# Performance work log

Hardware: AMD Instinct MI355X
Metric: run time of the kernel (lower is better)

The kernel has to match this reference:

```python
import jax, jax.numpy as jnp
import numpy as np

DIM = 1024
HEADS = 16
DIM_HEAD = 64
NUM_KV_HEADS = 4
INNER = HEADS * DIM_HEAD          # 1024
KV_DIM = NUM_KV_HEADS * DIM_HEAD  # 256
SCALE = DIM_HEAD ** -0.5


def setup_inputs() -> dict:
    key = jax.random.key(0)
    ks = jax.random.split(key, 7)
    B, S = 2, 2048
    x = jax.random.normal(ks[0], (B, S, DIM), dtype=jnp.float32)
    init = lambda k, shape: jax.random.normal(k, shape, dtype=jnp.float32) * (shape[0] ** -0.5)
    return {
        "x": x,
        "ln_gamma": jnp.ones((DIM,), jnp.float32),
        "ln_beta": jnp.zeros((DIM,), jnp.float32),
        "w_q": init(ks[1], (DIM, INNER)),
        "w_k": init(ks[2], (DIM, KV_DIM)),
        "w_v": init(ks[3], (DIM, KV_DIM)),
        "w_o": init(ks[4], (INNER, DIM)),
        "b_o": jnp.zeros((DIM,), jnp.float32),
    }


def reference(x, ln_gamma, ln_beta, w_q, w_k, w_v, w_o, b_o):
    B, S, _ = x.shape
    g, hpg, d = NUM_KV_HEADS, HEADS // NUM_KV_HEADS, DIM_HEAD
    # LayerNorm (eps matches torch default 1e-5)
    mu = jnp.mean(x, axis=-1, keepdims=True)
    var = jnp.mean((x - mu) ** 2, axis=-1, keepdims=True)
    xn = (x - mu) * jax.lax.rsqrt(var + 1e-5) * ln_gamma + ln_beta
    # projections
    q = xn @ w_q  # [B,S,INNER]
    k = xn @ w_k  # [B,S,KV_DIM]
    v = xn @ w_v
    # q: b s (g hpg d) -> b g hpg s d  (head index h = g*hpg + i, g-major)
    q = q.reshape(B, S, g, hpg, d).transpose(0, 2, 3, 1, 4)
    k = k.reshape(B, S, g, d).transpose(0, 2, 1, 3)  # [B,g,S,d]
    v = v.reshape(B, S, g, d).transpose(0, 2, 1, 3)
    dots = jnp.einsum('bghqd,bgkd->bghqk', q, k) * SCALE
    attn = jax.nn.softmax(dots, axis=-1)
    out = jnp.einsum('bghqk,bgkd->bghqd', attn, v)
    # b g hpg s d -> b s (g hpg d)
    out = out.transpose(0, 3, 1, 2, 4).reshape(B, S, INNER)
    return out @ w_o + b_o
```

## Files before the change

### kernel.cpp

```cpp
#include <hip/hip_runtime.h>

typedef unsigned short u16;
typedef __bf16 bf16x8 __attribute__((ext_vector_type(8)));
typedef short s16x4 __attribute__((ext_vector_type(4)));
typedef float f32x4 __attribute__((ext_vector_type(4)));

__device__ __forceinline__ unsigned f2u(float f) { union { float f; unsigned u; } v; v.f = f; return v.u; }
__device__ __forceinline__ float u2f(unsigned u) { union { unsigned u; float f; } v; v.u = u; return v.f; }

__device__ __forceinline__ u16 f32_to_bf16(float f) {
  unsigned u = f2u(f);
  return (u16)((u + 0x7FFFu + ((u >> 16) & 1u)) >> 16);
}
__device__ __forceinline__ unsigned pack_rnd(float a, float b) {
  unsigned ra = f2u(a), rb = f2u(b);
  ra = ra + 0x7FFFu + ((ra >> 16) & 1u);
  rb = (rb + 0x7FFFu + ((rb >> 16) & 1u)) & 0xFFFF0000u;
  return (ra >> 16) | rb;
}
__device__ __forceinline__ unsigned pack_trunc(float a, float b) {
#if __has_builtin(__builtin_amdgcn_perm)
  return __builtin_amdgcn_perm(f2u(b), f2u(a), 0x07060302u);
#else
  return (f2u(a) >> 16) | (f2u(b) & 0xFFFF0000u);
#endif
}
__device__ __forceinline__ unsigned perm_lo(unsigned a, unsigned b) {
#if __has_builtin(__builtin_amdgcn_perm)
  return __builtin_amdgcn_perm(b, a, 0x05040100u);
#else
  return (a & 0xFFFFu) | (b << 16);
#endif
}
__device__ __forceinline__ unsigned perm_hi(unsigned a, unsigned b) {
#if __has_builtin(__builtin_amdgcn_perm)
  return __builtin_amdgcn_perm(b, a, 0x07060302u);
#else
  return (a >> 16) | (b & 0xFFFF0000u);
#endif
}

#if __has_builtin(__builtin_amdgcn_global_load_lds)
#define ASYNC_CP 1
typedef __attribute__((address_space(1))) const unsigned gu32;
typedef __attribute__((address_space(3))) unsigned lu32;
__device__ __forceinline__ void gl_lds16(const u16* g, u16* l) {
  __builtin_amdgcn_global_load_lds((gu32*)g, (lu32*)l, 16, 0, 0);
}
#else
#define ASYNC_CP 0
#endif

__global__ __launch_bounds__(256) void prep_kernel(
    const float* __restrict__ x, const float* __restrict__ gamma,
    const float* __restrict__ beta, u16* __restrict__ xn,
    const float* __restrict__ w_q, const float* __restrict__ w_k,
    const float* __restrict__ w_v, const float* __restrict__ w_o,
    u16* __restrict__ wqkvT, u16* __restrict__ woT) {
  __shared__ float tile[64][65];
  int t = threadIdx.x;
  int bid = blockIdx.x;
  if (bid < 4096) {
    int row = bid;
    const float4 v = ((const float4*)(x + (size_t)row * 1024))[t];
    float s = v.x + v.y + v.z + v.w;
    float ss = v.x * v.x + v.y * v.y + v.z * v.z + v.w * v.w;
#pragma unroll
    for (int m = 1; m < 64; m <<= 1) {
      s += __shfl_xor(s, m, 64);
      ss += __shfl_xor(ss, m, 64);
    }
    __shared__ float as_[4], ass[4];
    int wave = t >> 6;
    if ((t & 63) == 0) { as_[wave] = s; ass[wave] = ss; }
    __syncthreads();
    s = as_[0] + as_[1] + as_[2] + as_[3];
    ss = ass[0] + ass[1] + ass[2] + ass[3];
    float mu = s * (1.0f / 1024.0f);
    float var = ss * (1.0f / 1024.0f) - mu * mu;
    float rstd = rsqrtf(var + 1e-5f);
    float4 g = ((const float4*)gamma)[t];
    float4 b = ((const float4*)beta)[t];
    uint2 o;
    o.x = pack_rnd((v.x - mu) * rstd * g.x + b.x, (v.y - mu) * rstd * g.y + b.y);
    o.y = pack_rnd((v.z - mu) * rstd * g.z + b.z, (v.w - mu) * rstd * g.w + b.w);
    ((uint2*)(xn + (size_t)row * 1024))[t] = o;
    return;
  }
  int idx = bid - 4096;
  const float* src; u16* dst; int N, n0, k0;
  if (idx < 256) {
    src = w_q; dst = wqkvT; N = 1024; n0 = (idx & 15) * 64; k0 = (idx >> 4) * 64;
  } else if (idx < 320) {
    int i = idx - 256;
    src = w_k; dst = wqkvT + 1024 * 1024; N = 256; n0 = (i & 3) * 64; k0 = (i >> 2) * 64;
  } else if (idx < 384) {
    int i = idx - 320;
    src = w_v; dst = wqkvT + 1280 * 1024; N = 256; n0 = (i & 3) * 64; k0 = (i >> 2) * 64;
  } else {
    int i = idx - 384;
    src = w_o; dst = woT; N = 1024; n0 = (i & 15) * 64; k0 = (i >> 4) * 64;
  }
  const int K = 1024;
  int c = t & 63, r4 = t >> 6;
#pragma unroll
  for (int rr = r4; rr < 64; rr += 4)
    tile[rr][c] = src[(size_t)(k0 + rr) * N + n0 + c];
  __syncthreads();
#pragma unroll
  for (int rr = r4; rr < 64; rr += 4)
    dst[(size_t)(n0 + rr) * K + k0 + c] = f32_to_bf16(tile[c][rr]);
}

template <int OUT_MODE>
__global__ __launch_bounds__(256) void gemm_bf16_k(
    const u16* __restrict__ A, const u16* __restrict__ Bt,
    void* __restrict__ Cv, const float* __restrict__ bias,
    int M, int N, int K, int ldc, float qscale, int qcols) {
  __shared__ __align__(16) u16 sA[64 * 64];
  __shared__ __align__(16) u16 sB[128 * 64];
  int t = threadIdx.x;
  int m0 = blockIdx.y * 64, n0 = blockIdx.x * 128;
  int wave = t >> 6, lane = t & 63;
  int wm = wave >> 1, wn = wave & 1;
  int l15 = lane & 15, quad = lane >> 4;

  f32x4 acc[2][4];
#pragma unroll
  for (int i = 0; i < 2; i++)
#pragma unroll
    for (int j = 0; j < 4; j++) acc[i][j] = f32x4{0.f, 0.f, 0.f, 0.f};

  int arow = wave * 8 + (lane >> 3);
  int achk = (lane & 7) * 8;
  const u16* Ap = A + (size_t)(m0 + arow) * K + achk;
  const u16* Bp = Bt + (size_t)(n0 + arow) * K + achk;
  u16* sAw = &sA[(wave * 8) * 64];
  u16* sBw = &sB[(wave * 8) * 64];

  for (int k0 = 0; k0 < K; k0 += 64) {
#if ASYNC_CP
    __syncthreads();
    gl_lds16(Ap + k0, sAw);
    gl_lds16(Ap + k0 + (size_t)32 * K, sAw + 32 * 64);
    gl_lds16(Bp + k0, sBw);
    gl_lds16(Bp + k0 + (size_t)32 * K, sBw + 32 * 64);
    gl_lds16(Bp + k0 + (size_t)64 * K, sBw + 64 * 64);
    gl_lds16(Bp + k0 + (size_t)96 * K, sBw + 96 * 64);
    __syncthreads();
#else
    uint4 av0 = *(const uint4*)(Ap + k0);
    uint4 av1 = *(const uint4*)(Ap + k0 + (size_t)32 * K);
    uint4 bv0 = *(const uint4*)(Bp + k0);
    uint4 bv1 = *(const uint4*)(Bp + k0 + (size_t)32 * K);
    uint4 bv2 = *(const uint4*)(Bp + k0 + (size_t)64 * K);
    uint4 bv3 = *(const uint4*)(Bp + k0 + (size_t)96 * K);
    __syncthreads();
    *(uint4*)&sA[arow * 64 + achk] = av0;
    *(uint4*)&sA[(arow + 32) * 64 + achk] = av1;
    *(uint4*)&sB[arow * 64 + achk] = bv0;
    *(uint4*)&sB[(arow + 32) * 64 + achk] = bv1;
    *(uint4*)&sB[(arow + 64) * 64 + achk] = bv2;
    *(uint4*)&sB[(arow + 96) * 64 + achk] = bv3;
    __syncthreads();
#endif
#pragma unroll
    for (int ks = 0; ks < 2; ++ks) {
      bf16x8 af[2], bf[4];
#pragma unroll
      for (int mi = 0; mi < 2; mi++)
        af[mi] = *(const bf16x8*)&sA[(wm * 32 + mi * 16 + l15) * 64 + ks * 32 + quad * 8];
#pragma unroll
      for (int ni = 0; ni < 4; ni++)
        bf[ni] = *(const bf16x8*)&sB[(wn * 64 + ni * 16 + l15) * 64 + ks * 32 + quad * 8];
#pragma unroll
      for (int mi = 0; mi < 2; mi++)
#pragma unroll
        for (int ni = 0; ni < 4; ni++)
          acc[mi][ni] = __builtin_amdgcn_mfma_f32_16x16x32_bf16(
              af[mi], bf[ni], acc[mi][ni], 0, 0, 0);
    }
  }
#pragma unroll
  for (int mi = 0; mi < 2; mi++)
#pragma unroll
    for (int ni = 0; ni < 4; ni++) {
      int row = m0 + wm * 32 + mi * 16 + quad * 4;
      int col = n0 + wn * 64 + ni * 16 + l15;
#pragma unroll
      for (int rr = 0; rr < 4; rr++) {
        float vv = acc[mi][ni][rr];
        if (OUT_MODE == 0) {
          float sc = (col < qcols) ? qscale : 1.0f;
          ((u16*)Cv)[(size_t)(row + rr) * ldc + col] = f32_to_bf16(vv * sc);
        } else {
          ((float*)Cv)[(size_t)(row + rr) * ldc + col] = vv + bias[col];
        }
      }
    }
}

__global__ __launch_bounds__(256) void attn_kernel(
    const u16* __restrict__ qkv, u16* __restrict__ oP0, u16* __restrict__ oP1,
    float* __restrict__ lP0, float* __restrict__ lP1) {
  const int LD = 1536;
  int qt = blockIdx.x;
  int bh = blockIdx.y;
  int kz = blockIdx.z;
  int b = bh >> 4, h = bh & 15, g = h >> 2;
  u16* oP = kz ? oP1 : oP0;
  float* lP = kz ? lP1 : lP0;

  __shared__ __align__(16) u16 sK[64 * 72];
  __shared__ __align__(16) u16 sV[64 * 72];

  int t = threadIdx.x, wave = t >> 6, lane = t & 63;
  int l15 = lane & 15, quad = lane >> 4;

  const u16* qbase = qkv + (size_t)(b * 2048 + qt * 256 + wave * 64) * LD + h * 64;
  const u16* kbase = qkv + (size_t)(b * 2048 + kz * 1024) * LD + 1024 + g * 64;
  const u16* vbase = kbase + 256;

  bf16x8 qf[4][2];
#pragma unroll
  for (int qs = 0; qs < 4; ++qs)
#pragma unroll
    for (int ks = 0; ks < 2; ++ks)
      qf[qs][ks] = *(const bf16x8*)(qbase + (size_t)(qs * 16 + l15) * LD + ks * 32 + quad * 8);

  f32x4 oacc[4][4];
  f32x4 lacc[4];
#pragma unroll
  for (int qs = 0; qs < 4; ++qs) {
    lacc[qs] = f32x4{0.f, 0.f, 0.f, 0.f};
#pragma unroll
    for (int md = 0; md < 4; ++md) oacc[qs][md] = f32x4{0.f, 0.f, 0.f, 0.f};
  }

  const s16x4 ones = {(short)0x3F80, (short)0x3F80, (short)0x3F80, (short)0x3F80};
  const f32x4 fzero = {0.f, 0.f, 0.f, 0.f};

  int sr = t >> 3, sq = t & 7;
  int vkp = (t & 31) * 2, vdc = (t >> 5) * 8;

  uint4 ka0, ka1, va0, va1;
  {
    const u16* kp0 = kbase + (size_t)sr * LD + sq * 8;
    ka0 = *(const uint4*)kp0;
    ka1 = *(const uint4*)(kp0 + (size_t)32 * LD);
    const u16* vp0 = vbase + (size_t)vkp * LD + vdc;
    va0 = *(const uint4*)vp0;
    va1 = *(const uint4*)(vp0 + LD);
  }

  for (int kt = 0; kt < 16; ++kt) {
    __syncthreads();
    *(uint4*)&sK[sr * 72 + sq * 8] = ka0;
    *(uint4*)&sK[(sr + 32) * 72 + sq * 8] = ka1;
    {
      const unsigned* aw = (const unsigned*)&va0;
      const unsigned* bw = (const unsigned*)&va1;
#pragma unroll
      for (int w = 0; w < 4; ++w) {
        *(unsigned*)&sV[(vdc + 2 * w) * 72 + vkp] = perm_lo(aw[w], bw[w]);
        *(unsigned*)&sV[(vdc + 2 * w + 1) * 72 + vkp] = perm_hi(aw[w], bw[w]);
      }
    }
    __syncthreads();

    if (kt < 15) {
      const u16* kp0 = kbase + (size_t)((kt + 1) * 64 + sr) * LD + sq * 8;
      ka0 = *(const uint4*)kp0;
      ka1 = *(const uint4*)(kp0 + (size_t)32 * LD);
      const u16* vp0 = vbase + (size_t)((kt + 1) * 64 + vkp) * LD + vdc;
      va0 = *(const uint4*)vp0;
      va1 = *(const uint4*)(vp0 + LD);
    }

    s16x4 pf[4][4];
#pragma unroll
    for (int ni = 0; ni < 4; ++ni) {
      bf16x8 kf0 = *(const bf16x8*)&sK[(ni * 16 + l15) * 72 + quad * 8];
      bf16x8 kf1 = *(const bf16x8*)&sK[(ni * 16 + l15) * 72 + 32 + quad * 8];
      f32x4 sacc[4];
#pragma unroll
      for (int qs = 0; qs < 4; ++qs)
        sacc[qs] = __builtin_amdgcn_mfma_f32_16x16x32_bf16(kf0, qf[qs][0], fzero, 0, 0, 0);
#pragma unroll
      for (int qs = 0; qs < 4; ++qs)
        sacc[qs] = __builtin_amdgcn_mfma_f32_16x16x32_bf16(kf1, qf[qs][1], sacc[qs], 0, 0, 0);
#pragma unroll
      for (int qs = 0; qs < 4; ++qs) {
        float p0 = __builtin_amdgcn_exp2f(sacc[qs][0]);
        float p1 = __builtin_amdgcn_exp2f(sacc[qs][1]);
        float p2 = __builtin_amdgcn_exp2f(sacc[qs][2]);
        float p3 = __builtin_amdgcn_exp2f(sacc[qs][3]);
        uint2 pk;
        pk.x = pack_trunc(p0, p1);
        pk.y = pack_trunc(p2, p3);
        pf[qs][ni] = *(s16x4*)&pk;
        lacc[qs] = __builtin_amdgcn_mfma_f32_16x16x16bf16_1k(ones, pf[qs][ni], lacc[qs], 0, 0, 0);
      }
    }

#pragma unroll
    for (int md = 0; md < 4; ++md)
#pragma unroll
      for (int ni = 0; ni < 4; ++ni) {
        s16x4 vf = *(const s16x4*)&sV[(md * 16 + l15) * 72 + ni * 16 + quad * 4];
#pragma unroll
        for (int qs = 0; qs < 4; ++qs)
          oacc[qs][md] = __builtin_amdgcn_mfma_f32_16x16x16bf16_1k(vf, pf[qs][ni], oacc[qs][md], 0, 0, 0);
      }
  }

#pragma unroll
  for (int qs = 0; qs < 4; ++qs) {
    int row = b * 2048 + qt * 256 + wave * 64 + qs * 16 + l15;
    u16* ob = oP + (size_t)row * 1024 + h * 64 + quad * 4;
#pragma unroll
    for (int md = 0; md < 4; ++md) {
      uint2 o;
      o.x = pack_rnd(oacc[qs][md][0], oacc[qs][md][1]);
      o.y = pack_rnd(oacc[qs][md][2], oacc[qs][md][3]);
      *(uint2*)(ob + md * 16) = o;
    }
    if (quad == 0) lP[row * 16 + h] = lacc[qs][0];
  }
}

__global__ __launch_bounds__(256) void attn_combine(
    const u16* __restrict__ oP0, u16* __restrict__ oP1_attn,
    const float* __restrict__ lP0, const float* __restrict__ lP1) {
  int t = threadIdx.x;
  int row = blockIdx.x * 2 + (t >> 7);
  int c8 = (t & 127) * 8;
  int h = c8 >> 6;
  float l = lP0[row * 16 + h] + lP1[row * 16 + h];
  float rinv = 1.0f / l;
  size_t off = (size_t)row * 1024 + c8;
  uint4 a = *(const uint4*)(oP0 + off);
  uint4 bb = *(const uint4*)(oP1_attn + off);
  const unsigned* aw = (const unsigned*)&a;
  const unsigned* bw = (const unsigned*)&bb;
  uint4 o;
  unsigned* ow = (unsigned*)&o;
#pragma unroll
  for (int i = 0; i < 4; ++i) {
    float x0 = u2f(aw[i] << 16) + u2f(bw[i] << 16);
    float x1 = u2f(aw[i] & 0xFFFF0000u) + u2f(bw[i] & 0xFFFF0000u);
    ow[i] = pack_rnd(x0 * rinv, x1 * rinv);
  }
  *(uint4*)(oP1_attn + off) = o;
}

extern "C" void kernel_launch(void* const* d_in, const int* in_sizes, int n_in,
                              void* d_out, int out_size, void* d_ws, size_t ws_size,
                              hipStream_t stream) {
  const float* x = (const float*)d_in[0];
  const float* gamma = (const float*)d_in[1];
  const float* beta = (const float*)d_in[2];
  const float* w_q = (const float*)d_in[3];
  const float* w_k = (const float*)d_in[4];
  const float* w_v = (const float*)d_in[5];
  const float* w_o = (const float*)d_in[6];
  const float* b_o = (const float*)d_in[7];
  float* out = (float*)d_out;

  char* ws = (char*)d_ws;
  u16* wqkvT = (u16*)ws;
  float* lP0 = (float*)ws;
  float* lP1 = (float*)(ws + 256u * 1024);
  u16* woT = (u16*)(ws + 3u * 1024 * 1024);
  u16* xn = (u16*)(ws + 5u * 1024 * 1024);
  u16* oP0 = xn;
  u16* qkv = (u16*)(ws + 13u * 1024 * 1024);
  u16* oP1 = (u16*)(ws + 25u * 1024 * 1024);

  const float cexp = 0.125f * 1.44269504088896f;

  prep_kernel<<<4736, 256, 0, stream>>>(x, gamma, beta, xn, w_q, w_k, w_v, w_o,
                                        wqkvT, woT);

  gemm_bf16_k<0><<<dim3(12, 64), 256, 0, stream>>>(xn, wqkvT, qkv, nullptr,
                                                   4096, 1536, 1024, 1536,
                                                   cexp, 1024);

  attn_kernel<<<dim3(8, 32, 2), 256, 0, stream>>>(qkv, oP0, oP1, lP0, lP1);
  attn_combine<<<dim3(2048), 256, 0, stream>>>(oP0, oP1, lP0, lP1);

  gemm_bf16_k<1><<<dim3(8, 64), 256, 0, stream>>>(oP1, woT, out, b_o,
                                                  4096, 1024, 1024, 1024,
                                                  1.0f, 0);
}
```

Before: 189.3 us.

## Fuse split-KV attention combine into the output projection GEMM A-tile load

Removes the separate attn_combine kernel. The output-projection GEMM now loads both partial attention outputs and their softmax denominators, merges and normalizes them in registers, and writes the bf16 result straight into the shared-memory A tile. The next K-slice's partials are prefetched after the barrier. This saves one launch and a full write and read of the combined activation, at the cost of reading two A sources, redoing the combine in each of the 8 N-column blocks, and higher register use in the GEMM.

```diff
diff --git a/kernel.cpp b/kernel.cpp
--- a/kernel.cpp
+++ b/kernel.cpp
@@ -112,11 +112,10 @@
     dst[(size_t)(n0 + rr) * K + k0 + c] = f32_to_bf16(tile[c][rr]);
 }
 
-template <int OUT_MODE>
-__global__ __launch_bounds__(256) void gemm_bf16_k(
+__global__ __launch_bounds__(256) void gemm_qkv_kernel(
     const u16* __restrict__ A, const u16* __restrict__ Bt,
-    void* __restrict__ Cv, const float* __restrict__ bias,
-    int M, int N, int K, int ldc, float qscale, int qcols) {
+    u16* __restrict__ Cv, int M, int N, int K, int ldc,
+    float qscale, int qcols) {
   __shared__ __align__(16) u16 sA[64 * 64];
   __shared__ __align__(16) u16 sB[128 * 64];
   int t = threadIdx.x;
@@ -187,16 +186,10 @@
     for (int ni = 0; ni < 4; ni++) {
       int row = m0 + wm * 32 + mi * 16 + quad * 4;
       int col = n0 + wn * 64 + ni * 16 + l15;
-#pragma unroll
-      for (int rr = 0; rr < 4; rr++) {
-        float vv = acc[mi][ni][rr];
-        if (OUT_MODE == 0) {
-          float sc = (col < qcols) ? qscale : 1.0f;
-          ((u16*)Cv)[(size_t)(row + rr) * ldc + col] = f32_to_bf16(vv * sc);
-        } else {
-          ((float*)Cv)[(size_t)(row + rr) * ldc + col] = vv + bias[col];
-        }
-      }
+      float sc = (col < qcols) ? qscale : 1.0f;
+#pragma unroll
+      for (int rr = 0; rr < 4; rr++)
+        Cv[(size_t)(row + rr) * ldc + col] = f32_to_bf16(acc[mi][ni][rr] * sc);
     }
 }
 
@@ -329,29 +322,124 @@
   }
 }
 
-__global__ __launch_bounds__(256) void attn_combine(
-    const u16* __restrict__ oP0, u16* __restrict__ oP1_attn,
-    const float* __restrict__ lP0, const float* __restrict__ lP1) {
+__global__ __launch_bounds__(256) void gemm_o_kernel(
+    const u16* __restrict__ oP0, const u16* __restrict__ oP1,
+    const float* __restrict__ lP0, const float* __restrict__ lP1,
+    const u16* __restrict__ Bt, float* __restrict__ C,
+    const float* __restrict__ bias) {
+  const int K = 1024, ldc = 1024;
+  __shared__ __align__(16) u16 sA[64 * 64];
+  __shared__ __align__(16) u16 sB[128 * 64];
   int t = threadIdx.x;
-  int row = blockIdx.x * 2 + (t >> 7);
-  int c8 = (t & 127) * 8;
-  int h = c8 >> 6;
-  float l = lP0[row * 16 + h] + lP1[row * 16 + h];
-  float rinv = 1.0f / l;
-  size_t off = (size_t)row * 1024 + c8;
-  uint4 a = *(const uint4*)(oP0 + off);
-  uint4 bb = *(const uint4*)(oP1_attn + off);
-  const unsigned* aw = (const unsigned*)&a;
-  const unsigned* bw = (const unsigned*)&bb;
-  uint4 o;
-  unsigned* ow = (unsigned*)&o;
-#pragma unroll
-  for (int i = 0; i < 4; ++i) {
-    float x0 = u2f(aw[i] << 16) + u2f(bw[i] << 16);
-    float x1 = u2f(aw[i] & 0xFFFF0000u) + u2f(bw[i] & 0xFFFF0000u);
-    ow[i] = pack_rnd(x0 * rinv, x1 * rinv);
-  }
-  *(uint4*)(oP1_attn + off) = o;
+  int m0 = blockIdx.y * 64, n0 = blockIdx.x * 128;
+  int wave = t >> 6, lane = t & 63;
+  int wm = wave >> 1, wn = wave & 1;
+  int l15 = lane & 15, quad = lane >> 4;
+
+  f32x4 acc[2][4];
+#pragma unroll
+  for (int i = 0; i < 2; i++)
+#pragma unroll
+    for (int j = 0; j < 4; j++) acc[i][j] = f32x4{0.f, 0.f, 0.f, 0.f};
+
+  int arow = wave * 8 + (lane >> 3);
+  int achk = (lane & 7) * 8;
+  int row0 = m0 + arow, row1 = row0 + 32;
+  const u16* Bp = Bt + (size_t)(n0 + arow) * K + achk;
+  u16* sBw = &sB[(wave * 8) * 64];
+
+  uint4 pa0, pa1, pb0, pb1;
+  float rin0, rin1;
+  {
+    size_t o0 = (size_t)row0 * 1024 + achk, o1 = (size_t)row1 * 1024 + achk;
+    pa0 = *(const uint4*)(oP0 + o0);
+    pb0 = *(const uint4*)(oP1 + o0);
+    pa1 = *(const uint4*)(oP0 + o1);
+    pb1 = *(const uint4*)(oP1 + o1);
+    rin0 = 1.0f / (lP0[row0 * 16] + lP1[row0 * 16]);
+    rin1 = 1.0f / (lP0[row1 * 16] + lP1[row1 * 16]);
+  }
+
+  for (int k0 = 0; k0 < K; k0 += 64) {
+    uint4 w0, w1;
+    {
+      const unsigned* a0 = (const unsigned*)&pa0;
+      const unsigned* b0 = (const unsigned*)&pb0;
+      const unsigned* a1 = (const unsigned*)&pa1;
+      const unsigned* b1 = (const unsigned*)&pb1;
+      unsigned* o0 = (unsigned*)&w0;
+      unsigned* o1 = (unsigned*)&w1;
+#pragma unroll
+      for (int i = 0; i < 4; ++i) {
+        float lo = u2f(a0[i] << 16) + u2f(b0[i] << 16);
+        float hi = u2f(a0[i] & 0xFFFF0000u) + u2f(b0[i] & 0xFFFF0000u);
+        o0[i] = pack_rnd(lo * rin0, hi * rin0);
+        lo = u2f(a1[i] << 16) + u2f(b1[i] << 16);
+        hi = u2f(a1[i] & 0xFFFF0000u) + u2f(b1[i] & 0xFFFF0000u);
+        o1[i] = pack_rnd(lo * rin1, hi * rin1);
+      }
+    }
+    __syncthreads();
+#if ASYNC_CP
+    gl_lds16(Bp + k0, sBw);
+    gl_lds16(Bp + k0 + (size_t)32 * K, sBw + 32 * 64);
+    gl_lds16(Bp + k0 + (size_t)64 * K, sBw + 64 * 64);
+    gl_lds16(Bp + k0 + (size_t)96 * K, sBw + 96 * 64);
+#else
+    {
+      uint4 bv0 = *(const uint4*)(Bp + k0);
+      uint4 bv1 = *(const uint4*)(Bp + k0 + (size_t)32 * K);
+      uint4 bv2 = *(const uint4*)(Bp + k0 + (size_t)64 * K);
+      uint4 bv3 = *(const uint4*)(Bp + k0 + (size_t)96 * K);
+      *(uint4*)&sB[arow * 64 + achk] = bv0;
+      *(uint4*)&sB[(arow + 32) * 64 + achk] = bv1;
+      *(uint4*)&sB[(arow + 64) * 64 + achk] = bv2;
+      *(uint4*)&sB[(arow + 96) * 64 + achk] = bv3;
+    }
+#endif
+    *(uint4*)&sA[arow * 64 + achk] = w0;
+    *(uint4*)&sA[(arow + 32) * 64 + achk] = w1;
+    __syncthreads();
+
+    if (k0 < K - 64) {
+      int h = (k0 >> 6) + 1;
+      size_t o0 = (size_t)row0 * 1024 + h * 64 + achk;
+      size_t o1 = (size_t)row1 * 1024 + h * 64 + achk;
+      pa0 = *(const uint4*)(oP0 + o0);
+      pb0 = *(const uint4*)(oP1 + o0);
+      pa1 = *(const uint4*)(oP0 + o1);
+      pb1 = *(const uint4*)(oP1 + o1);
+      rin0 = 1.0f / (lP0[row0 * 16 + h] + lP1[row0 * 16 + h]);
+      rin1 = 1.0f / (lP0[row1 * 16 + h] + lP1[row1 * 16 + h]);
+    }
+
+#pragma unroll
+    for (int ks = 0; ks < 2; ++ks) {
+      bf16x8 af[2], bf[4];
+#pragma unroll
+      for (int mi = 0; mi < 2; mi++)
+        af[mi] = *(const bf16x8*)&sA[(wm * 32 + mi * 16 + l15) * 64 + ks * 32 + quad * 8];
+#pragma unroll
+      for (int ni = 0; ni < 4; ni++)
+        bf[ni] = *(const bf16x8*)&sB[(wn * 64 + ni * 16 + l15) * 64 + ks * 32 + quad * 8];
+#pragma unroll
+      for (int mi = 0; mi < 2; mi++)
+#pragma unroll
+        for (int ni = 0; ni < 4; ni++)
+          acc[mi][ni] = __builtin_amdgcn_mfma_f32_16x16x32_bf16(
+              af[mi], bf[ni], acc[mi][ni], 0, 0, 0);
+    }
+  }
+#pragma unroll
+  for (int mi = 0; mi < 2; mi++)
+#pragma unroll
+    for (int ni = 0; ni < 4; ni++) {
+      int row = m0 + wm * 32 + mi * 16 + quad * 4;
+      int col = n0 + wn * 64 + ni * 16 + l15;
+#pragma unroll
+      for (int rr = 0; rr < 4; rr++)
+        C[(size_t)(row + rr) * ldc + col] = acc[mi][ni][rr] + bias[col];
+    }
 }
 
 extern "C" void kernel_launch(void* const* d_in, const int* in_sizes, int n_in,
@@ -382,14 +470,12 @@
   prep_kernel<<<4736, 256, 0, stream>>>(x, gamma, beta, xn, w_q, w_k, w_v, w_o,
                                         wqkvT, woT);
 
-  gemm_bf16_k<0><<<dim3(12, 64), 256, 0, stream>>>(xn, wqkvT, qkv, nullptr,
-                                                   4096, 1536, 1024, 1536,
-                                                   cexp, 1024);
+  gemm_qkv_kernel<<<dim3(12, 64), 256, 0, stream>>>(xn, wqkvT, qkv,
+                                                    4096, 1536, 1024, 1536,
+                                                    cexp, 1024);
 
   attn_kernel<<<dim3(8, 32, 2), 256, 0, stream>>>(qkv, oP0, oP1, lP0, lP1);
-  attn_combine<<<dim3(2048), 256, 0, stream>>>(oP0, oP1, lP0, lP1);
-
-  gemm_bf16_k<1><<<dim3(8, 64), 256, 0, stream>>>(oP1, woT, out, b_o,
-                                                  4096, 1024, 1024, 1024,
-                                                  1.0f, 0);
-}
+
+  gemm_o_kernel<<<dim3(8, 64), 256, 0, stream>>>(oP0, oP1, lP0, lP1,
+                                                 woT, out, b_o);
+}
```

Result: slower. 193.8 us (+2.4%).
